# Kernel tuning notes

Measured on AMD Instinct MI355X. Metric: run time of the kernel, lower is better.

The kernel has to match this reference:

```python
import jax, jax.numpy as jnp
import numpy as np

COMMITMENT_COST = 0.25  # hardcoded in VQVAEModel (quantizer commitment_cost=0.25)


def setup_inputs() -> dict:
    key = jax.random.key(0)
    k1, k2 = jax.random.split(key)
    B, D, H, W = 128, 64, 32, 32
    K = 512
    inputs = jax.random.normal(k1, (B, D, H, W), dtype=jnp.float32)
    codebook = jax.random.normal(k2, (K, D), dtype=jnp.float32)  # nn.Embedding weight, normal_()
    return {"inputs": inputs, "codebook": codebook}


def reference(inputs, codebook):
    # VectorQuantizerEMA.forward in eval mode (no EMA buffer update).
    B, D, H, W = inputs.shape
    K = codebook.shape[0]
    # BCHW -> BHWC
    x = jnp.transpose(inputs, (0, 2, 3, 1))
    flat = x.reshape(-1, D)  # [N, D], N = B*H*W
    distances = (jnp.sum(flat * flat, axis=1, keepdims=True)
                 + jnp.sum(codebook * codebook, axis=1)
                 - 2.0 * flat @ codebook.T)
    # max_one_hot(-distances) == one-hot of argmin(distances)
    idx = jnp.argmin(distances, axis=1)  # [N]
    oh = jax.nn.one_hot(idx, K, dtype=flat.dtype)  # [N, K]
    # quantized = onehot @ codebook (detached) == gather, same math, cheaper
    quantized = jax.lax.stop_gradient(codebook[idx]).reshape(x.shape)  # [B,H,W,D]
    # commitment loss (quantized is detached under torch.no_grad)
    e_latent_loss = jnp.mean((quantized - x) ** 2)
    loss = COMMITMENT_COST * e_latent_loss
    # straight-through estimator
    q_st = x + jax.lax.stop_gradient(quantized - x)
    # perplexity of codebook usage
    avg_probs = jnp.mean(oh, axis=0)
    perplexity = jnp.exp(-jnp.sum(avg_probs * jnp.log(avg_probs + 1e-10)))
    # oh_encodings: rearrange '(b n) d -> b d n'
    oh_encodings = jnp.transpose(oh.reshape(B, H * W, K), (0, 2, 1))  # [B, K, N]
    quantized_out = jnp.transpose(q_st, (0, 3, 1, 2))  # back to BCHW
    return loss, quantized_out, perplexity, oh_encodings
```

## Files before the change

### kernel.cpp

```cpp
#include <hip/hip_runtime.h>
#include <hip/hip_bf16.h>
#include <float.h>

#define NTOT 131072

#define OFF_LOSS  0
#define OFF_QUANT 1
#define OFF_PERP  8388609
#define OFF_OH    8388610

#define FLAG_BIT (1 << 16)
#define TAU      1.5e-3f
#define MAGIC    0x5EEDF00D
#define WSTRIDE  516

typedef __attribute__((ext_vector_type(8))) short short8;
typedef __attribute__((ext_vector_type(4))) short short4v;
typedef __attribute__((ext_vector_type(4))) float f32x4;

__device__ inline unsigned short f2bf(float f) {
    unsigned u = __builtin_bit_cast(unsigned, f);
    unsigned r = (u + 0x7fffu + ((u >> 16) & 1u)) >> 16;
    return (unsigned short)r;
}
__device__ inline float bf2f(unsigned short h) {
    return __builtin_bit_cast(float, ((unsigned)h) << 16);
}

__global__ __launch_bounds__(1024)
void vq_fused(const float* __restrict__ x, const float* __restrict__ cb,
              int* __restrict__ wsi, float* __restrict__ out) {
    __shared__ short Ehi[512 * 64];
    __shared__ short Elo[512 * 64];
    __shared__ float en_s[512];
    __shared__ float dist_s[512];
    __shared__ int   idx_s[512];
    __shared__ int   hist_s[512];

    const int t = threadIdx.x, wg = blockIdx.x;
    const int w = t >> 6, lane = t & 63;
    const int c = lane & 15, g = lane >> 4;
    const int b0 = wg >> 1;
    const int sphalf = (wg & 1) << 9;
    float* qout = out + OFF_QUANT;
    float* oh   = out + OFF_OH;

    if (t < 512) hist_s[t] = 0;

    const float4* cb4 = (const float4*)cb;
#pragma unroll
    for (int i = 0; i < 8; ++i) {
        int e4 = i * 1024 + t;
        float4 v = cb4[e4];
        int k = e4 >> 4, q = e4 & 15;
        int base = (k << 6) + ((((q >> 1) ^ (k & 7)) << 3) + ((q & 1) << 2));
        float vv[4] = {v.x, v.y, v.z, v.w};
        short4v h4, l4;
#pragma unroll
        for (int e = 0; e < 4; ++e) {
            unsigned short h = f2bf(vv[e]);
            h4[e] = (short)h;
            l4[e] = (short)f2bf(vv[e] - bf2f(h));
        }
        *(short4v*)&Ehi[base] = h4;
        *(short4v*)&Elo[base] = l4;
    }
    if (t < 512) {
        const float4* r4 = cb4 + (t << 4);
        float s = 0.f;
#pragma unroll
        for (int j = 0; j < 16; ++j) {
            float4 vv = r4[j];
            s = fmaf(vv.x, vv.x, s); s = fmaf(vv.y, vv.y, s);
            s = fmaf(vv.z, vv.z, s); s = fmaf(vv.w, vv.w, s);
        }
        en_s[t] = s;
    }

    short8 bh[2][2], bl[2][2];
    float xn2[2] = {0.f, 0.f};
    const float* xb = x + (((size_t)b0) << 16) + sphalf + (w << 5) + c;
#pragma unroll
    for (int xt = 0; xt < 2; ++xt) {
#pragma unroll
        for (int ks = 0; ks < 2; ++ks) {
            short8 h8, l8;
#pragma unroll
            for (int e = 0; e < 8; ++e) {
                float xv = xb[(xt << 4) + ((size_t)((ks << 5) + (g << 3) + e) << 10)];
                unsigned short hh = f2bf(xv);
                h8[e] = (short)hh;
                l8[e] = (short)f2bf(xv - bf2f(hh));
                xn2[xt] = fmaf(xv, xv, xn2[xt]);
            }
            bh[xt][ks] = h8; bl[xt][ks] = l8;
        }
    }
    float xnorm[2];
#pragma unroll
    for (int xt = 0; xt < 2; ++xt) {
        float v = xn2[xt];
        v += __shfl_xor(v, 16);
        v += __shfl_xor(v, 32);
        xnorm[xt] = v;
    }
    __syncthreads();

    float v1[2] = {FLT_MAX, FLT_MAX}, v2[2] = {FLT_MAX, FLT_MAX};
    int   i1[2] = {0, 0},            i2v[2] = {0, 0};
    const int sw = c & 7;
    const short* ph = &Ehi[c << 6];
    const short* pl = &Elo[c << 6];
#pragma unroll 2
    for (int kt = 0; kt < 32; ++kt) {
        const short* rh = ph + (kt << 10);
        const short* rl = pl + (kt << 10);
        short8 ah0 = *(const short8*)(rh + ((g ^ sw) << 3));
        short8 ah1 = *(const short8*)(rh + (((g + 4) ^ sw) << 3));
        short8 al0 = *(const short8*)(rl + ((g ^ sw) << 3));
        short8 al1 = *(const short8*)(rl + (((g + 4) ^ sw) << 3));
        float4 en4 = *(const float4*)&en_s[(kt << 4) + (g << 2)];
        float en_[4] = {en4.x, en4.y, en4.z, en4.w};
#pragma unroll
        for (int xt = 0; xt < 2; ++xt) {
            f32x4 acc = {0.f, 0.f, 0.f, 0.f};
            acc = __builtin_amdgcn_mfma_f32_16x16x32_bf16(ah0, bh[xt][0], acc, 0, 0, 0);
            acc = __builtin_amdgcn_mfma_f32_16x16x32_bf16(ah1, bh[xt][1], acc, 0, 0, 0);
            acc = __builtin_amdgcn_mfma_f32_16x16x32_bf16(al0, bh[xt][0], acc, 0, 0, 0);
            acc = __builtin_amdgcn_mfma_f32_16x16x32_bf16(al1, bh[xt][1], acc, 0, 0, 0);
            acc = __builtin_amdgcn_mfma_f32_16x16x32_bf16(ah0, bl[xt][0], acc, 0, 0, 0);
            acc = __builtin_amdgcn_mfma_f32_16x16x32_bf16(ah1, bl[xt][1], acc, 0, 0, 0);
#pragma unroll
            for (int r = 0; r < 4; ++r) {
                float dd = fmaf(-2.0f, acc[r], en_[r]);
                int k = (kt << 4) + (g << 2) + r;
                bool lt1 = dd < v1[xt];
                bool lt2 = dd < v2[xt];
                v2[xt] = lt1 ? v1[xt] : (lt2 ? dd : v2[xt]);
                i2v[xt] = lt1 ? i1[xt] : (lt2 ? k : i2v[xt]);
                v1[xt] = lt1 ? dd : v1[xt];
                i1[xt] = lt1 ? k : i1[xt];
            }
        }
    }

#pragma unroll
    for (int xt = 0; xt < 2; ++xt) {
        float V1 = v1[xt], V2 = v2[xt]; int I1 = i1[xt], I2 = i2v[xt];
#pragma unroll
        for (int off = 16; off <= 32; off <<= 1) {
            float o1 = __shfl_xor(V1, off); int oi1 = __shfl_xor(I1, off);
            float o2 = __shfl_xor(V2, off); int oi2 = __shfl_xor(I2, off);
            if (o1 < V1 || (o1 == V1 && oi1 < I1)) {
                V2 = V1; I2 = I1; V1 = o1; I1 = oi1;
            } else if (o1 < V2 || (o1 == V2 && oi1 < I2)) { V2 = o1; I2 = oi1; }
            if (o2 < V2 || (o2 == V2 && oi2 < I2)) { V2 = o2; I2 = oi2; }
        }
        if (g == 0) {
            int r = (w << 5) + (xt << 4) + c;
            idx_s[r]  = I1 | ((V2 - V1 < TAU) ? FLAG_BIT : 0);
            dist_s[r] = xnorm[xt] + V1;
        }
    }
    __syncthreads();

    {
        int full = idx_s[(w << 5) + (lane & 31)];
        unsigned long long m = __ballot((lane < 32) && (full & FLAG_BIT));
        while (m) {
            int r = __ffsll((long long)m) - 1; m &= m - 1;
            int sp = sphalf + (w << 5) + r;
            float xd = x[(((size_t)b0) << 16) + (((size_t)lane) << 10) + sp];
            double bestd = 1e300; int besti = 0x7fffffff;
            for (int kk = 0; kk < 8; ++kk) {
                int k = (lane << 3) + kk;
                const float* er = cb + (((size_t)k) << 6);
                double s = 0.0;
                for (int d = 0; d < 64; ++d) {
                    float xv = __shfl(xd, d);
                    double df = (double)xv - (double)er[d];
                    s = fma(df, df, s);
                }
                if (s < bestd || (s == bestd && k < besti)) { bestd = s; besti = k; }
            }
#pragma unroll
            for (int off = 32; off; off >>= 1) {
                double od = __shfl_xor(bestd, off);
                int    oi = __shfl_xor(besti, off);
                if (od < bestd || (od == bestd && oi < besti)) { bestd = od; besti = oi; }
            }
            if (lane == 0) {
                idx_s[(w << 5) + r]  = besti;
                dist_s[(w << 5) + r] = (float)bestd;
            }
        }
    }
    __syncthreads();

    if (t < 512) {
        int k = idx_s[t] & 511;
        idx_s[t] = k;
        atomicAdd(&hist_s[k], 1);
        float v = dist_s[t];
#pragma unroll
        for (int off = 1; off < 64; off <<= 1) v += __shfl_xor(v, off);
        if (lane == 0) en_s[w] = v;
    }
    __syncthreads();
    if (t < 512)
        __hip_atomic_store(&wsi[wg * WSTRIDE + t], hist_s[t],
                           __ATOMIC_RELAXED, __HIP_MEMORY_SCOPE_AGENT);
    if (t == 0) {
        float lsum = 0.f;
        for (int i = 0; i < 8; ++i) lsum += en_s[i];
        __hip_atomic_store(&wsi[wg * WSTRIDE + 512], __float_as_int(lsum),
                           __ATOMIC_RELAXED, __HIP_MEMORY_SCOPE_AGENT);
    }
    __syncthreads();
    if (t == 0)
        __hip_atomic_store(&wsi[wg * WSTRIDE + 513], MAGIC,
                           __ATOMIC_RELEASE, __HIP_MEMORY_SCOPE_AGENT);

    {
        const int pr = lane & 15, kk = lane >> 4;
        int2 iv = *(const int2*)&idx_s[(w << 5) + (pr << 1)];
        float* ohb = oh + (((size_t)b0) << 19) + sphalf + (w << 5) + (pr << 1);
#pragma unroll 4
        for (int kb = 0; kb < 512; kb += 4) {
            int k = kb + kk;
            float2 o;
            o.x = (iv.x == k) ? 1.f : 0.f;
            o.y = (iv.y == k) ? 1.f : 0.f;
            *(float2*)(ohb + (((size_t)k) << 10)) = o;
        }
    }
    {
        const int sp_l = lane & 31, dg = lane >> 5;
        int k = idx_s[(w << 5) + sp_l];
        const short* phq = &Ehi[k << 6];
        const short* plq = &Elo[k << 6];
        const int swq = k & 7;
        float* qb = qout + (((size_t)b0) << 16) + sphalf + (w << 5) + sp_l;
#pragma unroll
        for (int dblk = 0; dblk < 4; ++dblk) {
            int chunk = (dg << 2) + dblk;
            short8 h8 = *(const short8*)(phq + ((chunk ^ swq) << 3));
            short8 l8 = *(const short8*)(plq + ((chunk ^ swq) << 3));
#pragma unroll
            for (int e = 0; e < 8; ++e) {
                float v = bf2f((unsigned short)h8[e]) + bf2f((unsigned short)l8[e]);
                qb[((size_t)((dg << 5) + (dblk << 3) + e)) << 10] = v;
            }
        }
    }

    if (wg == 0) {
        if (t < 256) {
            while (__hip_atomic_load(&wsi[t * WSTRIDE + 513],
                                     __ATOMIC_ACQUIRE, __HIP_MEMORY_SCOPE_AGENT) != MAGIC)
                __builtin_amdgcn_s_sleep(2);
        }
        __syncthreads();
        float plog = 0.f, lpart = 0.f;
        if (t < 512) {
            int s = 0;
            for (int wgi = 0; wgi < 256; ++wgi)
                s += __hip_atomic_load(&wsi[wgi * WSTRIDE + t],
                                       __ATOMIC_RELAXED, __HIP_MEMORY_SCOPE_AGENT);
            float p = (float)s * (1.f / (float)NTOT);
            plog = p * logf(p + 1e-10f);
        }
        if (t < 256)
            lpart = __int_as_float(__hip_atomic_load(&wsi[t * WSTRIDE + 512],
                                       __ATOMIC_RELAXED, __HIP_MEMORY_SCOPE_AGENT));
#pragma unroll
        for (int off = 1; off < 64; off <<= 1) {
            plog  += __shfl_xor(plog, off);
            lpart += __shfl_xor(lpart, off);
        }
        __syncthreads();
        if (lane == 0 && w < 8) en_s[w] = plog;
        if (lane == 0 && w < 4) dist_s[w] = lpart;
        __syncthreads();
        if (t == 0) {
            float ps = 0.f; for (int i = 0; i < 8; ++i) ps += en_s[i];
            float ls = 0.f; for (int i = 0; i < 4; ++i) ls += dist_s[i];
            out[OFF_PERP] = expf(-ps);
            out[OFF_LOSS] = 0.25f * ls / ((float)NTOT * 64.0f);
        }
    }
}

extern "C" void kernel_launch(void* const* d_in, const int* in_sizes, int n_in,
                              void* d_out, int out_size, void* d_ws, size_t ws_size,
                              hipStream_t stream) {
    const float* x  = (const float*)d_in[0];
    const float* cb = (const float*)d_in[1];
    vq_fused<<<256, 1024, 0, stream>>>(x, cb, (int*)d_ws, (float*)d_out);
}
```

Baseline: 452.5 us.

## Remove block barriers via per-wave local reductions and last-wave publish

Drops three __syncthreads in the post-argmin phase. Each wave now handles its own rows for the histogram, and the loss is reduced through a shared atomic. A wave-counter lets the last wave publish the histogram, loss and flag to the workspace. The exact refine loop now reads the codebook as float4 with an unrolled inner loop, and the one-hot store loop uses pointer increments with deeper unrolling. The last-wave pattern depends on shared-memory atomics and fences for cross-wave visibility, which is a subtle correctness risk.

```diff
diff --git a/kernel.cpp b/kernel.cpp
--- a/kernel.cpp
+++ b/kernel.cpp
@@ -36,6 +36,8 @@
     __shared__ float dist_s[512];
     __shared__ int   idx_s[512];
     __shared__ int   hist_s[512];
+    __shared__ float loss_s;
+    __shared__ int   cnt_s;
 
     const int t = threadIdx.x, wg = blockIdx.x;
     const int w = t >> 6, lane = t & 63;
@@ -46,6 +48,7 @@
     float* oh   = out + OFF_OH;
 
     if (t < 512) hist_s[t] = 0;
+    if (t == 0) { loss_s = 0.f; cnt_s = 0; }
 
     const float4* cb4 = (const float4*)cb;
 #pragma unroll
@@ -162,11 +165,10 @@
             dist_s[r] = xnorm[xt] + V1;
         }
     }
-    __syncthreads();
 
     {
-        int full = idx_s[(w << 5) + (lane & 31)];
-        unsigned long long m = __ballot((lane < 32) && (full & FLAG_BIT));
+        int rowfull = (lane < 32) ? idx_s[(w << 5) + lane] : 0;
+        unsigned long long m = __ballot((lane < 32) && (rowfull & FLAG_BIT));
         while (m) {
             int r = __ffsll((long long)m) - 1; m &= m - 1;
             int sp = sphalf + (w << 5) + r;
@@ -174,12 +176,18 @@
             double bestd = 1e300; int besti = 0x7fffffff;
             for (int kk = 0; kk < 8; ++kk) {
                 int k = (lane << 3) + kk;
-                const float* er = cb + (((size_t)k) << 6);
                 double s = 0.0;
-                for (int d = 0; d < 64; ++d) {
-                    float xv = __shfl(xd, d);
-                    double df = (double)xv - (double)er[d];
-                    s = fma(df, df, s);
+#pragma unroll
+                for (int d4 = 0; d4 < 16; ++d4) {
+                    float4 e4 = cb4[(k << 4) + d4];
+                    float x0 = __shfl(xd, d4 * 4 + 0);
+                    float x1 = __shfl(xd, d4 * 4 + 1);
+                    float x2 = __shfl(xd, d4 * 4 + 2);
+                    float x3 = __shfl(xd, d4 * 4 + 3);
+                    double f0 = (double)x0 - (double)e4.x; s = fma(f0, f0, s);
+                    double f1 = (double)x1 - (double)e4.y; s = fma(f1, f1, s);
+                    double f2 = (double)x2 - (double)e4.z; s = fma(f2, f2, s);
+                    double f3 = (double)x3 - (double)e4.w; s = fma(f3, f3, s);
                 }
                 if (s < bestd || (s == bestd && k < besti)) { bestd = s; besti = k; }
             }
@@ -195,43 +203,51 @@
             }
         }
     }
-    __syncthreads();
-
-    if (t < 512) {
-        int k = idx_s[t] & 511;
-        idx_s[t] = k;
+
+    if (lane < 32) {
+        int r = (w << 5) + lane;
+        int k = idx_s[r] & 511;
+        idx_s[r] = k;
         atomicAdd(&hist_s[k], 1);
-        float v = dist_s[t];
-#pragma unroll
-        for (int off = 1; off < 64; off <<= 1) v += __shfl_xor(v, off);
-        if (lane == 0) en_s[w] = v;
-    }
-    __syncthreads();
-    if (t < 512)
-        __hip_atomic_store(&wsi[wg * WSTRIDE + t], hist_s[t],
-                           __ATOMIC_RELAXED, __HIP_MEMORY_SCOPE_AGENT);
-    if (t == 0) {
-        float lsum = 0.f;
-        for (int i = 0; i < 8; ++i) lsum += en_s[i];
-        __hip_atomic_store(&wsi[wg * WSTRIDE + 512], __float_as_int(lsum),
-                           __ATOMIC_RELAXED, __HIP_MEMORY_SCOPE_AGENT);
-    }
-    __syncthreads();
-    if (t == 0)
-        __hip_atomic_store(&wsi[wg * WSTRIDE + 513], MAGIC,
-                           __ATOMIC_RELEASE, __HIP_MEMORY_SCOPE_AGENT);
+    }
+    {
+        float lv = (lane < 32) ? dist_s[(w << 5) + lane] : 0.f;
+#pragma unroll
+        for (int off = 1; off < 64; off <<= 1) lv += __shfl_xor(lv, off);
+        if (lane == 0) atomicAdd(&loss_s, lv);
+    }
+    __threadfence_block();
+    int old16 = 0;
+    if (lane == 0) old16 = atomicAdd(&cnt_s, 1);
+    old16 = __shfl(old16, 0);
+    if (old16 == 15) {
+#pragma unroll
+        for (int j = 0; j < 8; ++j)
+            __hip_atomic_store(&wsi[wg * WSTRIDE + lane + (j << 6)],
+                               hist_s[lane + (j << 6)],
+                               __ATOMIC_RELAXED, __HIP_MEMORY_SCOPE_AGENT);
+        if (lane == 0)
+            __hip_atomic_store(&wsi[wg * WSTRIDE + 512], __float_as_int(loss_s),
+                               __ATOMIC_RELAXED, __HIP_MEMORY_SCOPE_AGENT);
+        __threadfence();
+        if (lane == 0)
+            __hip_atomic_store(&wsi[wg * WSTRIDE + 513], MAGIC,
+                               __ATOMIC_RELEASE, __HIP_MEMORY_SCOPE_AGENT);
+    }
 
     {
         const int pr = lane & 15, kk = lane >> 4;
         int2 iv = *(const int2*)&idx_s[(w << 5) + (pr << 1)];
-        float* ohb = oh + (((size_t)b0) << 19) + sphalf + (w << 5) + (pr << 1);
-#pragma unroll 4
+        float* p = oh + (((size_t)b0) << 19) + sphalf + (w << 5) + (pr << 1)
+                     + (((size_t)kk) << 10);
+#pragma unroll 8
         for (int kb = 0; kb < 512; kb += 4) {
             int k = kb + kk;
             float2 o;
             o.x = (iv.x == k) ? 1.f : 0.f;
             o.y = (iv.y == k) ? 1.f : 0.f;
-            *(float2*)(ohb + (((size_t)k) << 10)) = o;
+            *(float2*)p = o;
+            p += 4096;
         }
     }
     {
```

After: 538.4 us. +19.0%, slower.

## Coalesce one-hot and quantized output stores with row-contiguous float4 writes

Applied to the files above, without the earlier changes.

Replaces the per-position one-hot store loop with a row-wise float4 zero-fill of the workgroup's one-hot tile, followed by a scatter of the ones after a barrier. Reorganizes quantized output writes so each wave writes contiguous spatial runs of four dims with float4 stores, handling misaligned edge elements separately. Also unrolls and vectorizes codebook reads in the fp64 tie-break fallback. The goal is better write coalescing on the dominant output traffic, at the cost of an extra barrier, redundant writes where ones land, and gather-style reads of the codebook.

```diff
diff --git a/kernel.cpp b/kernel.cpp
--- a/kernel.cpp
+++ b/kernel.cpp
@@ -165,8 +165,8 @@
     __syncthreads();
 
     {
-        int full = idx_s[(w << 5) + (lane & 31)];
-        unsigned long long m = __ballot((lane < 32) && (full & FLAG_BIT));
+        int rowfull = (lane < 32) ? idx_s[(w << 5) + lane] : 0;
+        unsigned long long m = __ballot((lane < 32) && (rowfull & FLAG_BIT));
         while (m) {
             int r = __ffsll((long long)m) - 1; m &= m - 1;
             int sp = sphalf + (w << 5) + r;
@@ -174,12 +174,18 @@
             double bestd = 1e300; int besti = 0x7fffffff;
             for (int kk = 0; kk < 8; ++kk) {
                 int k = (lane << 3) + kk;
-                const float* er = cb + (((size_t)k) << 6);
                 double s = 0.0;
-                for (int d = 0; d < 64; ++d) {
-                    float xv = __shfl(xd, d);
-                    double df = (double)xv - (double)er[d];
-                    s = fma(df, df, s);
+#pragma unroll
+                for (int d4 = 0; d4 < 16; ++d4) {
+                    float4 e4 = cb4[(k << 4) + d4];
+                    float x0 = __shfl(xd, d4 * 4 + 0);
+                    float x1 = __shfl(xd, d4 * 4 + 1);
+                    float x2 = __shfl(xd, d4 * 4 + 2);
+                    float x3 = __shfl(xd, d4 * 4 + 3);
+                    double f0 = (double)x0 - (double)e4.x; s = fma(f0, f0, s);
+                    double f1 = (double)x1 - (double)e4.y; s = fma(f1, f1, s);
+                    double f2 = (double)x2 - (double)e4.z; s = fma(f2, f2, s);
+                    double f3 = (double)x3 - (double)e4.w; s = fma(f3, f3, s);
                 }
                 if (s < bestd || (s == bestd && k < besti)) { bestd = s; besti = k; }
             }
@@ -222,34 +228,61 @@
                            __ATOMIC_RELEASE, __HIP_MEMORY_SCOPE_AGENT);
 
     {
-        const int pr = lane & 15, kk = lane >> 4;
-        int2 iv = *(const int2*)&idx_s[(w << 5) + (pr << 1)];
-        float* ohb = oh + (((size_t)b0) << 19) + sphalf + (w << 5) + (pr << 1);
-#pragma unroll 4
-        for (int kb = 0; kb < 512; kb += 4) {
-            int k = kb + kk;
-            float2 o;
-            o.x = (iv.x == k) ? 1.f : 0.f;
-            o.y = (iv.y == k) ? 1.f : 0.f;
-            *(float2*)(ohb + (((size_t)k) << 10)) = o;
-        }
-    }
+        float4 z4 = {0.f, 0.f, 0.f, 0.f};
+        float2 z2 = {0.f, 0.f};
+        float* base_wg = oh + (((size_t)b0) << 19) + sphalf;
+        for (int j = 0; j < 32; ++j) {
+            int k = w + (j << 4);
+            float* cbase = base_wg + (((size_t)k) << 10);
+            *(float4*)(cbase + 2 + (lane << 2)) = z4;
+            if (lane < 63)
+                *(float4*)(cbase + 2 + ((64 + lane) << 2)) = z4;
+            else {
+                *(float2*)(cbase)       = z2;
+                *(float2*)(cbase + 510) = z2;
+            }
+        }
+    }
+    __syncthreads();
+
+    if (t < 512) {
+        int k = idx_s[t];
+        oh[(((size_t)b0) << 19) + (((size_t)k) << 10) + sphalf + t] = 1.0f;
+    }
+
     {
-        const int sp_l = lane & 31, dg = lane >> 5;
-        int k = idx_s[(w << 5) + sp_l];
-        const short* phq = &Ehi[k << 6];
-        const short* plq = &Elo[k << 6];
-        const int swq = k & 7;
-        float* qb = qout + (((size_t)b0) << 16) + sphalf + (w << 5) + sp_l;
-#pragma unroll
-        for (int dblk = 0; dblk < 4; ++dblk) {
-            int chunk = (dg << 2) + dblk;
-            short8 h8 = *(const short8*)(phq + ((chunk ^ swq) << 3));
-            short8 l8 = *(const short8*)(plq + ((chunk ^ swq) << 3));
-#pragma unroll
-            for (int e = 0; e < 8; ++e) {
-                float v = bf2f((unsigned short)h8[e]) + bf2f((unsigned short)l8[e]);
-                qb[((size_t)((dg << 5) + (dblk << 3) + e)) << 10] = v;
+        float* qbase = qout + (((size_t)b0) << 16) + sphalf;
+#pragma unroll
+        for (int j = 0; j < 4; ++j) {
+            int d = (w << 2) + j;
+            const int ch = d >> 3, dj = d & 7;
+            float* rb = qbase + (((size_t)d) << 10);
+#pragma unroll
+            for (int rnd = 0; rnd < 2; ++rnd) {
+                int m = (rnd << 6) + lane;
+                if (m < 127) {
+                    int s0 = 3 + (m << 2);
+                    float vv[4];
+#pragma unroll
+                    for (int e = 0; e < 4; ++e) {
+                        int k = idx_s[s0 + e];
+                        int a = (k << 6) + (((ch ^ (k & 7)) << 3) + dj);
+                        vv[e] = bf2f((unsigned short)Ehi[a]) + bf2f((unsigned short)Elo[a]);
+                    }
+                    float4 v4 = {vv[0], vv[1], vv[2], vv[3]};
+                    *(float4*)(rb + s0) = v4;
+                } else if (rnd == 1) {
+                    int k0 = idx_s[0], k1 = idx_s[1], k2 = idx_s[2], k5 = idx_s[511];
+                    int a0 = (k0 << 6) + (((ch ^ (k0 & 7)) << 3) + dj);
+                    int a1 = (k1 << 6) + (((ch ^ (k1 & 7)) << 3) + dj);
+                    int a2 = (k2 << 6) + (((ch ^ (k2 & 7)) << 3) + dj);
+                    int a5 = (k5 << 6) + (((ch ^ (k5 & 7)) << 3) + dj);
+                    rb[0] = bf2f((unsigned short)Ehi[a0]) + bf2f((unsigned short)Elo[a0]);
+                    float2 e2 = { bf2f((unsigned short)Ehi[a1]) + bf2f((unsigned short)Elo[a1]),
+                                  bf2f((unsigned short)Ehi[a2]) + bf2f((unsigned short)Elo[a2]) };
+                    *(float2*)(rb + 1) = e2;
+                    rb[511] = bf2f((unsigned short)Ehi[a5]) + bf2f((unsigned short)Elo[a5]);
+                }
             }
         }
     }
```

New measurement: 417.6 us. 1.08x faster.
